# Kernel tuning notes

Hardware: AMD Instinct MI355X
Metric: run time of the kernel (lower is better)

Reference implementation:

```python
import jax, jax.numpy as jnp
import numpy as np


def setup_inputs() -> dict:
    key = jax.random.key(0)
    k1, k2 = jax.random.split(key)
    B, Q, T, D = 128, 512, 512, 256
    inputs = jax.random.normal(k1, (B, T, D), dtype=jnp.float32)
    query = jax.random.normal(k2, (B, Q, D), dtype=jnp.float32)
    return {"inputs": inputs, "query": query}


def reference(inputs, query):
    # inputs: [B, T, D] (keys == values), query: [B, Q, D]
    D = inputs.shape[2]
    scale = 1.0 / jnp.sqrt(jnp.asarray(D, dtype=inputs.dtype))
    # scores: [B, Q, T]
    scores = jnp.einsum("bqd,btd->bqt", query, inputs) * scale
    weights = jax.nn.softmax(scores, axis=2)
    # attended: [B, Q, D]
    attended = jnp.einsum("bqt,btd->bqd", weights, inputs)
    # pool over query dim -> [B, D]
    return jnp.sum(attended, axis=1)
```

## Files before the change

### kernel.cpp

```cpp
#include <hip/hip_runtime.h>
#include <hip/hip_bf16.h>


typedef __bf16 bf16x8 __attribute__((ext_vector_type(8)));
typedef float  f32x4  __attribute__((ext_vector_type(4)));

#define B_    128
#define Qn    512
#define Tn    512
#define Dn    256
#define QB    64
#define SCALE 0.0625f

__device__ __forceinline__ int sw_idx(int row, int ch) {
  return row * 256 + ((ch ^ (row & 7)) << 3);
}

__device__ __forceinline__ void stage_tile(const float* __restrict__ src,
                                           __bf16* dst, int tid) {
#pragma unroll
  for (int i = 0; i < 8; ++i) {
    int u = i * 256 + tid;
    int row = u >> 5;
    int ch  = u & 31;
    const float4* p = (const float4*)(src + row * 256 + ch * 8);
    float4 v0 = p[0];
    float4 v1 = p[1];
    bf16x8 w;
    w[0] = (__bf16)v0.x; w[1] = (__bf16)v0.y;
    w[2] = (__bf16)v0.z; w[3] = (__bf16)v0.w;
    w[4] = (__bf16)v1.x; w[5] = (__bf16)v1.y;
    w[6] = (__bf16)v1.z; w[7] = (__bf16)v1.w;
    *(bf16x8*)(dst + sw_idx(row, ch)) = w;
  }
}

__global__ void __launch_bounds__(256, 2) attn_qk_colsum(
    const float* __restrict__ inputs, const float* __restrict__ query,
    float* __restrict__ c_ws) {
  __shared__ __bf16 smem[2 * 64 * 256];
  __bf16* Qs = smem;
  __bf16* Ks = smem + 64 * 256;
  float* cpart = (float*)smem;

  int tid  = threadIdx.x;
  int bidx = blockIdx.x;
  int b  = bidx & 127;
  int qt = bidx >> 7;

  const float* qsrc = query  + ((size_t)b * Qn + (size_t)qt * QB) * Dn;
  const float* ksrc = inputs + (size_t)b * Tn * Dn;

  stage_tile(qsrc, Qs, tid);

  int wave = tid >> 6;
  int lane = tid & 63;
  int quad = lane >> 4;
  int l15  = lane & 15;

  f32x4 acc[32];
  f32x4 zero = {0.f, 0.f, 0.f, 0.f};
#pragma unroll
  for (int i = 0; i < 32; ++i) acc[i] = zero;

  int arow = wave * 16 + l15;

#pragma unroll
  for (int tt = 0; tt < 8; ++tt) {
    __syncthreads();
    stage_tile(ksrc + (size_t)tt * 64 * Dn, Ks, tid);
    __syncthreads();
#pragma unroll
    for (int dc = 0; dc < 8; ++dc) {
      bf16x8 a = *(const bf16x8*)(Qs + sw_idx(arow, dc * 4 + quad));
#pragma unroll
      for (int ct = 0; ct < 4; ++ct) {
        bf16x8 kb = *(const bf16x8*)(Ks + sw_idx(ct * 16 + l15, dc * 4 + quad));
        acc[tt * 4 + ct] =
            __builtin_amdgcn_mfma_f32_16x16x32_bf16(a, kb, acc[tt * 4 + ct], 0, 0, 0);
      }
    }
  }

  float mrow[4], lrow[4];
#pragma unroll
  for (int r = 0; r < 4; ++r) mrow[r] = -1e30f;
#pragma unroll
  for (int i = 0; i < 32; ++i)
#pragma unroll
    for (int r = 0; r < 4; ++r) mrow[r] = fmaxf(mrow[r], acc[i][r]);
#pragma unroll
  for (int off = 1; off <= 8; off <<= 1)
#pragma unroll
    for (int r = 0; r < 4; ++r) mrow[r] = fmaxf(mrow[r], __shfl_xor(mrow[r], off));
#pragma unroll
  for (int r = 0; r < 4; ++r) { mrow[r] *= SCALE; lrow[r] = 0.f; }
#pragma unroll
  for (int i = 0; i < 32; ++i)
#pragma unroll
    for (int r = 0; r < 4; ++r) {
      float p = __expf(acc[i][r] * SCALE - mrow[r]);
      acc[i][r] = p;
      lrow[r] += p;
    }
#pragma unroll
  for (int off = 1; off <= 8; off <<= 1)
#pragma unroll
    for (int r = 0; r < 4; ++r) lrow[r] += __shfl_xor(lrow[r], off);
  float inv[4];
#pragma unroll
  for (int r = 0; r < 4; ++r) inv[r] = 1.f / lrow[r];

  __syncthreads();

#pragma unroll
  for (int i = 0; i < 32; ++i) {
    float v = acc[i][0] * inv[0] + acc[i][1] * inv[1] +
              acc[i][2] * inv[2] + acc[i][3] * inv[3];
    v += __shfl_xor(v, 16);
    v += __shfl_xor(v, 32);
    if (lane < 16) {
      int t = (i >> 2) * 64 + (i & 3) * 16 + l15;
      cpart[wave * 512 + t] = v;
    }
  }
  __syncthreads();

  float* cout = c_ws + ((size_t)qt * B_ + b) * Tn;
#pragma unroll
  for (int t = tid; t < 512; t += 256)
    cout[t] = cpart[t] + cpart[512 + t] + cpart[1024 + t] + cpart[1536 + t];
}

__global__ void __launch_bounds__(512) attn_av(
    const float* __restrict__ inputs, const float* __restrict__ c_ws,
    float* __restrict__ out) {
  __shared__ float ctot[512];
  __shared__ float psum[256];
  int b = blockIdx.x;
  int tid = threadIdx.x;

  {
    float s = 0.f;
#pragma unroll
    for (int q = 0; q < 8; ++q) s += c_ws[((size_t)q * B_ + b) * Tn + tid];
    ctot[tid] = s;
  }
  __syncthreads();

  int d    = tid & 255;
  int half = tid >> 8;
  const float* vbase = inputs + ((size_t)b * Tn + (size_t)half * 256) * Dn + d;
  const float* cw = ctot + half * 256;
  float o = 0.f;
#pragma unroll 8
  for (int t = 0; t < 256; ++t) o += cw[t] * vbase[(size_t)t * 256];

  if (half) psum[d] = o;
  __syncthreads();
  if (!half) out[b * 256 + d] = o + psum[d];
}

extern "C" void kernel_launch(void* const* d_in, const int* in_sizes, int n_in,
                              void* d_out, int out_size, void* d_ws, size_t ws_size,
                              hipStream_t stream) {
  const float* inputs = (const float*)d_in[0];
  const float* query  = (const float*)d_in[1];
  float* out  = (float*)d_out;
  float* c_ws = (float*)d_ws;

  attn_qk_colsum<<<dim3(1024), dim3(256), 0, stream>>>(inputs, query, c_ws);
  attn_av<<<dim3(128), dim3(512), 0, stream>>>(inputs, c_ws, out);
}
```

Measured before the change: 189.4 us.

## Pre-convert keys to swizzled bf16 image and stream with async LDS double buffering

A new prep kernel converts the inputs once into a swizzled bf16 image in workspace. The QK kernel then streams K tiles straight into LDS with global_load_lds into double buffers, keeps Q fragments in registers, and uses 128-query blocks of 8 waves. The AV kernel reads the bf16 image split over two T halves and combines them with atomicAdd after a memset. The softmax drops the max subtraction, which risks overflow for large scores, and the bf16 V adds rounding error.

After: 190.4 us. Within noise of the previous version (+0.6%).

```diff
diff --git a/kernel.cpp b/kernel.cpp
--- a/kernel.cpp
+++ b/kernel.cpp
@@ -6,159 +6,191 @@
 typedef float  f32x4  __attribute__((ext_vector_type(4)));
 
 #define B_    128
-#define Qn    512
 #define Tn    512
 #define Dn    256
-#define QB    64
 #define SCALE 0.0625f
-
-__device__ __forceinline__ int sw_idx(int row, int ch) {
-  return row * 256 + ((ch ^ (row & 7)) << 3);
-}
-
-__device__ __forceinline__ void stage_tile(const float* __restrict__ src,
-                                           __bf16* dst, int tid) {
+#define IMG_BYTES ((size_t)B_ * 8 * 32768)
+
+__device__ __forceinline__ int gpos(int row, int ch) {
+  return row * 32 + ((ch ^ row) & 31);
+}
+
+__device__ __forceinline__ void async_copy16(void* lds, const void* g) {
+  __builtin_amdgcn_global_load_lds(
+      (const __attribute__((address_space(1))) unsigned int*)g,
+      (__attribute__((address_space(3))) unsigned int*)lds, 16, 0, 0);
+}
+
+__global__ void __launch_bounds__(256) prep(const float* __restrict__ inputs,
+                                            __bf16* __restrict__ img) {
+  const int bid = blockIdx.x;
+  const int b = bid & 127, tt = bid >> 7;
+  const int tid = threadIdx.x;
+  const float* src = inputs + ((size_t)b * Tn + (size_t)tt * 64) * Dn;
+  __bf16* dst = img + ((size_t)(b * 8 + tt)) * 16384;
 #pragma unroll
   for (int i = 0; i < 8; ++i) {
-    int u = i * 256 + tid;
-    int row = u >> 5;
-    int ch  = u & 31;
+    int g = i * 256 + tid;
+    int row = g >> 5, pos = g & 31;
+    int ch = (pos ^ row) & 31;
     const float4* p = (const float4*)(src + row * 256 + ch * 8);
-    float4 v0 = p[0];
-    float4 v1 = p[1];
+    float4 v0 = p[0], v1 = p[1];
     bf16x8 w;
     w[0] = (__bf16)v0.x; w[1] = (__bf16)v0.y;
     w[2] = (__bf16)v0.z; w[3] = (__bf16)v0.w;
     w[4] = (__bf16)v1.x; w[5] = (__bf16)v1.y;
     w[6] = (__bf16)v1.z; w[7] = (__bf16)v1.w;
-    *(bf16x8*)(dst + sw_idx(row, ch)) = w;
-  }
-}
-
-__global__ void __launch_bounds__(256, 2) attn_qk_colsum(
-    const float* __restrict__ inputs, const float* __restrict__ query,
+    *(bf16x8*)(dst + (size_t)g * 8) = w;
+  }
+}
+
+__global__ void __launch_bounds__(512, 2) attn_qk(
+    const __bf16* __restrict__ img, const float* __restrict__ query,
     float* __restrict__ c_ws) {
-  __shared__ __bf16 smem[2 * 64 * 256];
-  __bf16* Qs = smem;
-  __bf16* Ks = smem + 64 * 256;
-  float* cpart = (float*)smem;
-
-  int tid  = threadIdx.x;
-  int bidx = blockIdx.x;
-  int b  = bidx & 127;
-  int qt = bidx >> 7;
-
-  const float* qsrc = query  + ((size_t)b * Qn + (size_t)qt * QB) * Dn;
-  const float* ksrc = inputs + (size_t)b * Tn * Dn;
-
-  stage_tile(qsrc, Qs, tid);
-
-  int wave = tid >> 6;
-  int lane = tid & 63;
-  int quad = lane >> 4;
-  int l15  = lane & 15;
-
-  f32x4 acc[32];
+  __shared__ __bf16 Kb[2][64 * 256];
+
+  const int tid  = threadIdx.x;
+  const int bidx = blockIdx.x;
+  const int b  = bidx & 127;
+  const int qt = bidx >> 7;
+
+  const float*  qsrc = query + ((size_t)b * 512 + (size_t)qt * 128) * Dn;
+  const __bf16* kimg = img + (size_t)b * 8 * 16384;
+
+  const int wave = tid >> 6, lane = tid & 63;
+  const int quad = lane >> 4, l15 = lane & 15;
+
+#pragma unroll
+  for (int i = 0; i < 4; ++i) {
+    int off = (wave * 4 + i) * 512 + lane * 8;
+    async_copy16((void*)((__bf16*)Kb[0] + off), (const void*)(kimg + off));
+  }
+
+  bf16x8 afrag[8];
+#pragma unroll
+  for (int dc = 0; dc < 8; ++dc) {
+    const float4* p =
+        (const float4*)(qsrc + (wave * 16 + l15) * 256 + dc * 32 + quad * 8);
+    float4 v0 = p[0], v1 = p[1];
+    bf16x8 w;
+    w[0] = (__bf16)v0.x; w[1] = (__bf16)v0.y;
+    w[2] = (__bf16)v0.z; w[3] = (__bf16)v0.w;
+    w[4] = (__bf16)v1.x; w[5] = (__bf16)v1.y;
+    w[6] = (__bf16)v1.z; w[7] = (__bf16)v1.w;
+    afrag[dc] = w;
+  }
+  __syncthreads();
+
+  f32x4 acc[8][4];
   f32x4 zero = {0.f, 0.f, 0.f, 0.f};
 #pragma unroll
-  for (int i = 0; i < 32; ++i) acc[i] = zero;
-
-  int arow = wave * 16 + l15;
+  for (int tt = 0; tt < 8; ++tt)
+#pragma unroll
+    for (int ct = 0; ct < 4; ++ct) acc[tt][ct] = zero;
 
 #pragma unroll
   for (int tt = 0; tt < 8; ++tt) {
-    __syncthreads();
-    stage_tile(ksrc + (size_t)tt * 64 * Dn, Ks, tid);
-    __syncthreads();
-#pragma unroll
-    for (int dc = 0; dc < 8; ++dc) {
-      bf16x8 a = *(const bf16x8*)(Qs + sw_idx(arow, dc * 4 + quad));
-#pragma unroll
-      for (int ct = 0; ct < 4; ++ct) {
-        bf16x8 kb = *(const bf16x8*)(Ks + sw_idx(ct * 16 + l15, dc * 4 + quad));
-        acc[tt * 4 + ct] =
-            __builtin_amdgcn_mfma_f32_16x16x32_bf16(a, kb, acc[tt * 4 + ct], 0, 0, 0);
+    if (tt < 7) {
+      const __bf16* nsrc = kimg + (size_t)(tt + 1) * 16384;
+      __bf16* ndst = (__bf16*)Kb[(tt + 1) & 1];
+#pragma unroll
+      for (int i = 0; i < 4; ++i) {
+        int off = (wave * 4 + i) * 512 + lane * 8;
+        async_copy16((void*)(ndst + off), (const void*)(nsrc + off));
       }
     }
-  }
-
-  float mrow[4], lrow[4];
-#pragma unroll
-  for (int r = 0; r < 4; ++r) mrow[r] = -1e30f;
-#pragma unroll
-  for (int i = 0; i < 32; ++i)
-#pragma unroll
-    for (int r = 0; r < 4; ++r) mrow[r] = fmaxf(mrow[r], acc[i][r]);
+    const __bf16* cur = Kb[tt & 1];
+#pragma unroll
+    for (int dc = 0; dc < 8; ++dc) {
+#pragma unroll
+      for (int ct = 0; ct < 4; ++ct) {
+        bf16x8 bb =
+            *(const bf16x8*)(cur + gpos(ct * 16 + l15, dc * 4 + quad) * 8);
+        acc[tt][ct] = __builtin_amdgcn_mfma_f32_16x16x32_bf16(
+            afrag[dc], bb, acc[tt][ct], 0, 0, 0);
+      }
+    }
+    __syncthreads();
+  }
+
+  float rs[4] = {0.f, 0.f, 0.f, 0.f};
+#pragma unroll
+  for (int tt = 0; tt < 8; ++tt)
+#pragma unroll
+    for (int ct = 0; ct < 4; ++ct)
+#pragma unroll
+      for (int r = 0; r < 4; ++r) {
+        float p = __expf(acc[tt][ct][r] * SCALE);
+        acc[tt][ct][r] = p;
+        rs[r] += p;
+      }
 #pragma unroll
   for (int off = 1; off <= 8; off <<= 1)
 #pragma unroll
-    for (int r = 0; r < 4; ++r) mrow[r] = fmaxf(mrow[r], __shfl_xor(mrow[r], off));
-#pragma unroll
-  for (int r = 0; r < 4; ++r) { mrow[r] *= SCALE; lrow[r] = 0.f; }
-#pragma unroll
-  for (int i = 0; i < 32; ++i)
-#pragma unroll
-    for (int r = 0; r < 4; ++r) {
-      float p = __expf(acc[i][r] * SCALE - mrow[r]);
-      acc[i][r] = p;
-      lrow[r] += p;
+    for (int r = 0; r < 4; ++r) rs[r] += __shfl_xor(rs[r], off);
+  float linv[4];
+#pragma unroll
+  for (int r = 0; r < 4; ++r) linv[r] = 1.f / rs[r];
+
+  float* cpart = (float*)Kb;
+#pragma unroll
+  for (int tt = 0; tt < 8; ++tt)
+#pragma unroll
+    for (int ct = 0; ct < 4; ++ct) {
+      float v = acc[tt][ct][0] * linv[0] + acc[tt][ct][1] * linv[1] +
+                acc[tt][ct][2] * linv[2] + acc[tt][ct][3] * linv[3];
+      v += __shfl_xor(v, 16);
+      v += __shfl_xor(v, 32);
+      if (quad == 0) cpart[wave * 512 + tt * 64 + ct * 16 + l15] = v;
     }
-#pragma unroll
-  for (int off = 1; off <= 8; off <<= 1)
-#pragma unroll
-    for (int r = 0; r < 4; ++r) lrow[r] += __shfl_xor(lrow[r], off);
-  float inv[4];
-#pragma unroll
-  for (int r = 0; r < 4; ++r) inv[r] = 1.f / lrow[r];
-
-  __syncthreads();
-
-#pragma unroll
-  for (int i = 0; i < 32; ++i) {
-    float v = acc[i][0] * inv[0] + acc[i][1] * inv[1] +
-              acc[i][2] * inv[2] + acc[i][3] * inv[3];
-    v += __shfl_xor(v, 16);
-    v += __shfl_xor(v, 32);
-    if (lane < 16) {
-      int t = (i >> 2) * 64 + (i & 3) * 16 + l15;
-      cpart[wave * 512 + t] = v;
-    }
-  }
-  __syncthreads();
-
-  float* cout = c_ws + ((size_t)qt * B_ + b) * Tn;
-#pragma unroll
-  for (int t = tid; t < 512; t += 256)
-    cout[t] = cpart[t] + cpart[512 + t] + cpart[1024 + t] + cpart[1536 + t];
-}
-
-__global__ void __launch_bounds__(512) attn_av(
-    const float* __restrict__ inputs, const float* __restrict__ c_ws,
+  __syncthreads();
+
+  float csum = 0.f;
+#pragma unroll
+  for (int w = 0; w < 8; ++w) csum += cpart[w * 512 + tid];
+  c_ws[((size_t)qt * B_ + b) * Tn + tid] = csum;
+}
+
+__global__ void __launch_bounds__(256) attn_av(
+    const __bf16* __restrict__ img, const float* __restrict__ c_ws,
     float* __restrict__ out) {
-  __shared__ float ctot[512];
-  __shared__ float psum[256];
-  int b = blockIdx.x;
-  int tid = threadIdx.x;
+  __shared__ float cs[256];
+  __shared__ float psum[4][256];
+  const int bid = blockIdx.x;
+  const int b = bid & 127, th = bid >> 7;
+  const int tid = threadIdx.x;
+  const int wave = tid >> 6, lane = tid & 63;
+  const int ch = lane & 31, phase = lane >> 5;
 
   {
-    float s = 0.f;
-#pragma unroll
-    for (int q = 0; q < 8; ++q) s += c_ws[((size_t)q * B_ + b) * Tn + tid];
-    ctot[tid] = s;
-  }
-  __syncthreads();
-
-  int d    = tid & 255;
-  int half = tid >> 8;
-  const float* vbase = inputs + ((size_t)b * Tn + (size_t)half * 256) * Dn + d;
-  const float* cw = ctot + half * 256;
-  float o = 0.f;
-#pragma unroll 8
-  for (int t = 0; t < 256; ++t) o += cw[t] * vbase[(size_t)t * 256];
-
-  if (half) psum[d] = o;
-  __syncthreads();
-  if (!half) out[b * 256 + d] = o + psum[d];
+    int t = th * 256 + tid;
+    cs[tid] = c_ws[(size_t)(0 * B_ + b) * Tn + t] +
+              c_ws[(size_t)(1 * B_ + b) * Tn + t] +
+              c_ws[(size_t)(2 * B_ + b) * Tn + t] +
+              c_ws[(size_t)(3 * B_ + b) * Tn + t];
+  }
+  __syncthreads();
+
+  const __bf16* tile = img + (size_t)(b * 8 + th * 4 + wave) * 16384;
+  float o[8] = {0.f, 0.f, 0.f, 0.f, 0.f, 0.f, 0.f, 0.f};
+#pragma unroll
+  for (int j = 0; j < 32; ++j) {
+    int row = j * 2 + phase;
+    float c = cs[wave * 64 + row];
+    bf16x8 v = *(const bf16x8*)(tile + gpos(row, ch) * 8);
+#pragma unroll
+    for (int k = 0; k < 8; ++k) o[k] += c * (float)v[k];
+  }
+#pragma unroll
+  for (int k = 0; k < 8; ++k) o[k] += __shfl_xor(o[k], 32);
+  if (phase == 0) {
+#pragma unroll
+    for (int k = 0; k < 8; ++k) psum[wave][ch * 8 + k] = o[k];
+  }
+  __syncthreads();
+
+  float s = psum[0][tid] + psum[1][tid] + psum[2][tid] + psum[3][tid];
+  atomicAdd(out + b * 256 + tid, s);
 }
 
 extern "C" void kernel_launch(void* const* d_in, const int* in_sizes, int n_in,
@@ -166,9 +198,12 @@
                               hipStream_t stream) {
   const float* inputs = (const float*)d_in[0];
   const float* query  = (const float*)d_in[1];
-  float* out  = (float*)d_out;
-  float* c_ws = (float*)d_ws;
-
-  attn_qk_colsum<<<dim3(1024), dim3(256), 0, stream>>>(inputs, query, c_ws);
-  attn_av<<<dim3(128), dim3(512), 0, stream>>>(inputs, c_ws, out);
-}
+  float* out = (float*)d_out;
+  __bf16* img = (__bf16*)d_ws;
+  float* c_ws = (float*)((char*)d_ws + IMG_BYTES);
+
+  hipMemsetAsync(out, 0, (size_t)B_ * Dn * sizeof(float), stream);
+  prep<<<dim3(1024), dim3(256), 0, stream>>>(inputs, img);
+  attn_qk<<<dim3(512), dim3(512), 0, stream>>>(img, query, c_ws);
+  attn_av<<<dim3(256), dim3(256), 0, stream>>>(img, c_ws, out);
+}
```
